# Kernel optimization log

Hardware: AMD Instinct MI355X
Metric: run time of the kernel (lower is better)

Reference implementation:

```python
import jax, jax.numpy as jnp
import numpy as np

# AntModel forward, expressed at the ant-count level.
# Original: builds per-batch ragged routing tables where every ant at source
# neuron s is routed by the layer to a destination neuron; counts at each
# destination are accumulated, relu'd, and destinations with zero ants are
# pruned from the table (a no-op on the count vector itself). The deterministic
# layer routing used here is dest[s] = argmax(weights[s, :]).

B = 256
DIMS = [(4096, 4096), (4096, 4096), (4096, 1024)]
MAX_ANTS = 8


def setup_inputs() -> dict:
    key = jax.random.key(0)
    kx, k1, k2, k3 = jax.random.split(key, 4)
    x = jax.random.randint(kx, (B, DIMS[0][0]), 0, MAX_ANTS).astype(jnp.int32)
    W1 = jax.random.normal(k1, DIMS[0], dtype=jnp.float32)
    W2 = jax.random.normal(k2, DIMS[1], dtype=jnp.float32)
    W3 = jax.random.normal(k3, DIMS[2], dtype=jnp.float32)
    return {"x": x, "W1": W1, "W2": W2, "W3": W3}


def _layer(counts, W):
    # counts: [B, n_in] int32 ant counts; W: [n_in, n_out] pheromone weights
    dest = jnp.argmax(W, axis=1)  # [n_in] routing table
    n_out = W.shape[1]
    out = jnp.zeros((counts.shape[0], n_out), dtype=counts.dtype)
    out = out.at[:, dest].add(counts)  # scatter-add counts to destinations
    return jnp.maximum(out, 0)  # layer.relu_func (identity on counts)


def reference(x, W1, W2, W3):
    counts = x.astype(jnp.int32)
    for W in (W1, W2, W3):
        counts = _layer(counts, W)
    return counts.astype(jnp.float32)
```

## Files before the change

kernel.cpp:

```cpp
#include <hip/hip_runtime.h>


#define N_IN   4096
#define N_MID  4096
#define N_OUT  1024
#define BATCH  256

__device__ __forceinline__ void upd(float v, int idx, float& bv, int& bi) {
    if (v > bv || (v == bv && idx < bi)) { bv = v; bi = idx; }
}

template <int NCOLS>
__device__ __forceinline__ void row_argmax(const float* __restrict__ W, int row,
                                           int* __restrict__ dest) {
    const int lane = threadIdx.x & 63;
    const float4* __restrict__ p =
        reinterpret_cast<const float4*>(W + (size_t)row * NCOLS);
    float bv = -__builtin_huge_valf();
    int bi = 0;
    #pragma unroll
    for (int t = 0; t < NCOLS / 256; ++t) {
        float4 v = p[(size_t)t * 64 + lane];
        int c = t * 256 + lane * 4;
        upd(v.x, c + 0, bv, bi);
        upd(v.y, c + 1, bv, bi);
        upd(v.z, c + 2, bv, bi);
        upd(v.w, c + 3, bv, bi);
    }
    #pragma unroll
    for (int off = 1; off < 64; off <<= 1) {
        float ov = __shfl_xor(bv, off, 64);
        int   oi = __shfl_xor(bi, off, 64);
        if (ov > bv || (ov == bv && oi < bi)) { bv = ov; bi = oi; }
    }
    if (lane == 0) dest[row] = bi;
}

__global__ __launch_bounds__(256) void argmax_all_kernel(
    const float* __restrict__ W1, const float* __restrict__ W2,
    const float* __restrict__ W3, int* __restrict__ dest1,
    int* __restrict__ dest2, int* __restrict__ dest3) {
    const int wave = (blockIdx.x * blockDim.x + threadIdx.x) >> 6;
    if (wave < N_IN) {
        row_argmax<N_MID>(W1, wave, dest1);
    } else if (wave < N_IN + N_MID) {
        row_argmax<N_MID>(W2, wave - N_IN, dest2);
    } else {
        row_argmax<N_OUT>(W3, wave - (N_IN + N_MID), dest3);
    }
}

__global__ __launch_bounds__(256) void compose_kernel(
    const int* __restrict__ dest1, const int* __restrict__ dest2,
    const int* __restrict__ dest3, int* __restrict__ fdest) {
    const int s = blockIdx.x * blockDim.x + threadIdx.x;
    if (s < N_IN) fdest[s] = dest3[dest2[dest1[s]]];
}

__global__ __launch_bounds__(256) void scatter_kernel(
    const int* __restrict__ x, const int* __restrict__ fdest,
    float* __restrict__ out) {
    __shared__ int cnt[N_OUT];
    const int b = blockIdx.x;
    for (int i = threadIdx.x; i < N_OUT; i += 256) cnt[i] = 0;
    __syncthreads();
    const int* __restrict__ xb = x + (size_t)b * N_IN;
    const int4* __restrict__ x4 = reinterpret_cast<const int4*>(xb);
    for (int q = threadIdx.x; q < N_IN / 4; q += 256) {
        int4 v = x4[q];
        int s = q * 4;
        atomicAdd(&cnt[fdest[s + 0]], v.x);
        atomicAdd(&cnt[fdest[s + 1]], v.y);
        atomicAdd(&cnt[fdest[s + 2]], v.z);
        atomicAdd(&cnt[fdest[s + 3]], v.w);
    }
    __syncthreads();
    float* __restrict__ ob = out + (size_t)b * N_OUT;
    for (int i = threadIdx.x; i < N_OUT; i += 256) ob[i] = (float)cnt[i];
}

extern "C" void kernel_launch(void* const* d_in, const int* in_sizes, int n_in,
                              void* d_out, int out_size, void* d_ws, size_t ws_size,
                              hipStream_t stream) {
    const int*   x  = (const int*)d_in[0];
    const float* W1 = (const float*)d_in[1];
    const float* W2 = (const float*)d_in[2];
    const float* W3 = (const float*)d_in[3];
    float* out = (float*)d_out;

    int* ws    = (int*)d_ws;
    int* dest1 = ws;
    int* dest2 = ws + N_IN;
    int* dest3 = ws + 2 * N_IN;
    int* fdest = ws + 3 * N_IN;

    const int total_waves = N_IN + N_MID + N_MID;
    argmax_all_kernel<<<total_waves / 4, 256, 0, stream>>>(W1, W2, W3,
                                                           dest1, dest2, dest3);
    compose_kernel<<<N_IN / 256, 256, 0, stream>>>(dest1, dest2, dest3, fdest);
    scatter_kernel<<<BATCH, 256, 0, stream>>>(x, fdest, out);
}
```

Before: 170.6 us.

## Balance argmax work across waves and fuse route composition into scatter

Every wave now handles one W1/W2 row plus a half-row slice of W3. The W3 halves are merged through a 64-bit packed atomicMax on an order-preserving float key. Each wave's W1/W2 column chunks start at a phase that depends on the row, to spread memory accesses, and loads are issued in two batches of eight float4 for more memory-level parallelism. The compose kernel is removed: each scatter block rebuilds the full routing table in shared memory. This adds a memset launch and recomputes the composition 256 times, in exchange for one fewer launch and balanced wave work.

```diff
diff --git a/kernel.cpp b/kernel.cpp
--- a/kernel.cpp
+++ b/kernel.cpp
@@ -6,73 +6,122 @@
 #define N_OUT  1024
 #define BATCH  256
 
+using u32 = unsigned int;
+using u64 = unsigned long long;
+
+__device__ __forceinline__ u32 forder(float f) {
+    u32 b = __float_as_uint(f);
+    return (b & 0x80000000u) ? ~b : (b | 0x80000000u);
+}
+
 __device__ __forceinline__ void upd(float v, int idx, float& bv, int& bi) {
     if (v > bv || (v == bv && idx < bi)) { bv = v; bi = idx; }
 }
 
-template <int NCOLS>
-__device__ __forceinline__ void row_argmax(const float* __restrict__ W, int row,
-                                           int* __restrict__ dest) {
-    const int lane = threadIdx.x & 63;
-    const float4* __restrict__ p =
-        reinterpret_cast<const float4*>(W + (size_t)row * NCOLS);
-    float bv = -__builtin_huge_valf();
-    int bi = 0;
-    #pragma unroll
-    for (int t = 0; t < NCOLS / 256; ++t) {
-        float4 v = p[(size_t)t * 64 + lane];
-        int c = t * 256 + lane * 4;
-        upd(v.x, c + 0, bv, bi);
-        upd(v.y, c + 1, bv, bi);
-        upd(v.z, c + 2, bv, bi);
-        upd(v.w, c + 3, bv, bi);
-    }
+__device__ __forceinline__ void wave_reduce(float& bv, int& bi) {
     #pragma unroll
     for (int off = 1; off < 64; off <<= 1) {
         float ov = __shfl_xor(bv, off, 64);
         int   oi = __shfl_xor(bi, off, 64);
         if (ov > bv || (ov == bv && oi < bi)) { bv = ov; bi = oi; }
     }
-    if (lane == 0) dest[row] = bi;
 }
 
-__global__ __launch_bounds__(256) void argmax_all_kernel(
+__global__ __launch_bounds__(256) void argmax_fused_kernel(
     const float* __restrict__ W1, const float* __restrict__ W2,
     const float* __restrict__ W3, int* __restrict__ dest1,
-    int* __restrict__ dest2, int* __restrict__ dest3) {
-    const int wave = (blockIdx.x * blockDim.x + threadIdx.x) >> 6;
-    if (wave < N_IN) {
-        row_argmax<N_MID>(W1, wave, dest1);
-    } else if (wave < N_IN + N_MID) {
-        row_argmax<N_MID>(W2, wave - N_IN, dest2);
-    } else {
-        row_argmax<N_OUT>(W3, wave - (N_IN + N_MID), dest3);
+    int* __restrict__ dest2, u64* __restrict__ packed3) {
+    const int g    = (blockIdx.x * 256 + (int)threadIdx.x) >> 6;
+    const int lane = threadIdx.x & 63;
+
+    const int rowB = g & (N_IN - 1);
+    const float4* __restrict__ pb = reinterpret_cast<const float4*>(
+        ((g < N_IN) ? W1 : W2) + (size_t)rowB * N_MID);
+    const int phase = g & 15;
+
+    const int row3  = g >> 1;
+    const int cbase = (g & 1) * 2;
+    const float4* __restrict__ p3 =
+        reinterpret_cast<const float4*>(W3 + (size_t)row3 * N_OUT);
+
+    float4 va[8];
+    int ca[8];
+    #pragma unroll
+    for (int j = 0; j < 8; ++j) {
+        ca[j] = (j + phase) & 15;
+        va[j] = pb[ca[j] * 64 + lane];
+    }
+    float4 v3[2];
+    v3[0] = p3[(cbase + 0) * 64 + lane];
+    v3[1] = p3[(cbase + 1) * 64 + lane];
+
+    float bv = -__builtin_huge_valf(); int bi = 0;
+    #pragma unroll
+    for (int j = 0; j < 8; ++j) {
+        const int c = ca[j] * 256 + lane * 4;
+        upd(va[j].x, c + 0, bv, bi);
+        upd(va[j].y, c + 1, bv, bi);
+        upd(va[j].z, c + 2, bv, bi);
+        upd(va[j].w, c + 3, bv, bi);
+    }
+    float4 vb[8];
+    int cb[8];
+    #pragma unroll
+    for (int j = 0; j < 8; ++j) {
+        cb[j] = (j + 8 + phase) & 15;
+        vb[j] = pb[cb[j] * 64 + lane];
+    }
+    #pragma unroll
+    for (int j = 0; j < 8; ++j) {
+        const int c = cb[j] * 256 + lane * 4;
+        upd(vb[j].x, c + 0, bv, bi);
+        upd(vb[j].y, c + 1, bv, bi);
+        upd(vb[j].z, c + 2, bv, bi);
+        upd(vb[j].w, c + 3, bv, bi);
+    }
+    wave_reduce(bv, bi);
+    if (lane == 0) ((g < N_IN) ? dest1 : dest2)[rowB] = bi;
+
+    float b3 = -__builtin_huge_valf(); int i3 = 0;
+    #pragma unroll
+    for (int t = 0; t < 2; ++t) {
+        const int c = (cbase + t) * 256 + lane * 4;
+        upd(v3[t].x, c + 0, b3, i3);
+        upd(v3[t].y, c + 1, b3, i3);
+        upd(v3[t].z, c + 2, b3, i3);
+        upd(v3[t].w, c + 3, b3, i3);
+    }
+    wave_reduce(b3, i3);
+    if (lane == 0) {
+        u64 key = ((u64)forder(b3) << 32) | (u32)(~(u32)i3);
+        atomicMax(&packed3[row3], key);
     }
 }
 
-__global__ __launch_bounds__(256) void compose_kernel(
-    const int* __restrict__ dest1, const int* __restrict__ dest2,
-    const int* __restrict__ dest3, int* __restrict__ fdest) {
-    const int s = blockIdx.x * blockDim.x + threadIdx.x;
-    if (s < N_IN) fdest[s] = dest3[dest2[dest1[s]]];
-}
-
-__global__ __launch_bounds__(256) void scatter_kernel(
-    const int* __restrict__ x, const int* __restrict__ fdest,
+__global__ __launch_bounds__(256) void scatter_fused_kernel(
+    const int* __restrict__ x, const int* __restrict__ dest1,
+    const int* __restrict__ dest2, const u64* __restrict__ packed3,
     float* __restrict__ out) {
+    __shared__ int fd[N_IN];
     __shared__ int cnt[N_OUT];
     const int b = blockIdx.x;
+    for (int s = threadIdx.x; s < N_IN; s += 256) {
+        int d1 = dest1[s];
+        int d2 = dest2[d1];
+        u64 p  = packed3[d2];
+        fd[s]  = (int)(~(u32)p);
+    }
     for (int i = threadIdx.x; i < N_OUT; i += 256) cnt[i] = 0;
     __syncthreads();
-    const int* __restrict__ xb = x + (size_t)b * N_IN;
-    const int4* __restrict__ x4 = reinterpret_cast<const int4*>(xb);
+    const int4* __restrict__ x4 =
+        reinterpret_cast<const int4*>(x + (size_t)b * N_IN);
     for (int q = threadIdx.x; q < N_IN / 4; q += 256) {
         int4 v = x4[q];
         int s = q * 4;
-        atomicAdd(&cnt[fdest[s + 0]], v.x);
-        atomicAdd(&cnt[fdest[s + 1]], v.y);
-        atomicAdd(&cnt[fdest[s + 2]], v.z);
-        atomicAdd(&cnt[fdest[s + 3]], v.w);
+        atomicAdd(&cnt[fd[s + 0]], v.x);
+        atomicAdd(&cnt[fd[s + 1]], v.y);
+        atomicAdd(&cnt[fd[s + 2]], v.z);
+        atomicAdd(&cnt[fd[s + 3]], v.w);
     }
     __syncthreads();
     float* __restrict__ ob = out + (size_t)b * N_OUT;
@@ -88,15 +137,13 @@
     const float* W3 = (const float*)d_in[3];
     float* out = (float*)d_out;
 
-    int* ws    = (int*)d_ws;
-    int* dest1 = ws;
-    int* dest2 = ws + N_IN;
-    int* dest3 = ws + 2 * N_IN;
-    int* fdest = ws + 3 * N_IN;
+    u64* packed3 = (u64*)d_ws;
+    int* dest1   = (int*)(packed3 + N_MID);
+    int* dest2   = dest1 + N_IN;
 
-    const int total_waves = N_IN + N_MID + N_MID;
-    argmax_all_kernel<<<total_waves / 4, 256, 0, stream>>>(W1, W2, W3,
-                                                           dest1, dest2, dest3);
-    compose_kernel<<<N_IN / 256, 256, 0, stream>>>(dest1, dest2, dest3, fdest);
-    scatter_kernel<<<BATCH, 256, 0, stream>>>(x, fdest, out);
+    hipMemsetAsync(packed3, 0, N_MID * sizeof(u64), stream);
+    argmax_fused_kernel<<<(N_IN + N_MID) / 4, 256, 0, stream>>>(
+        W1, W2, W3, dest1, dest2, packed3);
+    scatter_fused_kernel<<<BATCH, 256, 0, stream>>>(x, dest1, dest2, packed3,
+                                                    out);
 }
```

Measured after the change: 184.5 us. 8.2% more time.
